# Performance work log

Measured on AMD Instinct MI355X. Metric: run time of the kernel, lower is better.

## Reference

```python
import jax, jax.numpy as jnp
import numpy as np
import itertools


def _interpn_linear(vol, loc):
    """Trilinear interpolation of vol [D,H,W,C] at absolute coords loc [D,H,W,3].
    Matches neurite's interpn: clip coords to volume, floor/ceil corners, 8-corner
    weighted sum (nearest-extrapolation at borders)."""
    D, H, W, C = vol.shape
    max_idx = jnp.asarray([D - 1, H - 1, W - 1], dtype=loc.dtype)
    loc = jnp.clip(loc, 0.0, max_idx)
    loc0 = jnp.floor(loc)
    loc1 = jnp.minimum(loc0 + 1.0, max_idx)
    d1 = loc1 - loc                     # weight of corner 0 (floor)
    d0 = 1.0 - d1                       # weight of corner 1 (ceil)
    w = jnp.stack([d1, d0], axis=0)     # [2, D,H,W,3]
    idx = jnp.stack([loc0, loc1], axis=0).astype(jnp.int32)  # [2, D,H,W,3]
    vol_flat = vol.reshape(-1, C)
    out = jnp.zeros(loc.shape[:-1] + (C,), vol.dtype)
    for c in itertools.product((0, 1), repeat=3):  # fixed 8-corner loop
        flat = (idx[c[0], ..., 0] * H + idx[c[1], ..., 1]) * W + idx[c[2], ..., 2]
        wt = w[c[0], ..., 0] * w[c[1], ..., 1] * w[c[2], ..., 2]
        out = out + wt[..., None] * vol_flat[flat]
    return out


def _warp(vol, shift):
    """Sample dense field vol [D,H,W,3] at grid + shift (voxelmorph transform())."""
    D, H, W, _ = shift.shape
    grid = jnp.stack(
        jnp.meshgrid(jnp.arange(D), jnp.arange(H), jnp.arange(W), indexing='ij'),
        axis=-1,
    ).astype(shift.dtype)
    return _interpn_linear(vol, grid + shift)


def _compose(transforms):
    """voxelmorph utils.compose for dense transforms: T(x) = C(B(A(x))).
    curr = curr + warp(nxt, curr), folding right-to-left."""
    curr = transforms[-1]
    for nxt in reversed(transforms[:-1]):
        curr = curr + jax.vmap(_warp)(nxt, curr)
    return curr


def setup_inputs() -> dict:
    key = jax.random.key(0)
    k1, k2, k3 = jax.random.split(key, 3)
    shape = (2, 128, 160, 192, 3)  # [B, D, H, W, ndims] dense displacement fields
    scale = 3.0  # ~3-voxel displacements, realistic registration magnitude
    return {
        't1': scale * jax.random.normal(k1, shape, dtype=jnp.float32),
        't2': scale * jax.random.normal(k2, shape, dtype=jnp.float32),
        't3': scale * jax.random.normal(k3, shape, dtype=jnp.float32),
    }


def reference(t1, t2, t3):
    # Transforms listed in application order A, B, C -> T(x) = C(B(A(x)))
    return _compose([t1, t2, t3])
```

## Files before the change

### kernel.cpp

```cpp
#include <hip/hip_runtime.h>
#include <hip/hip_fp16.h>


#define BB 2
#define DD 128
#define HH 160
#define WW 192

#define WT_TILES 3
#define HT_TILES 80
#define DT_TILES 64
#define NBLOCKS (WT_TILES * HT_TILES * DT_TILES * BB)
#define PER_XCD (NBLOCKS / 8)

static __device__ __forceinline__ float3 cvt_h4(uint2 q) {
    float2 fa = __half22float2(*(const __half2*)&q.x);
    float  fz = __half2float(*(const __half*)&q.y);
    return make_float3(fa.x, fa.y, fz);
}

__global__ __launch_bounds__(256) void conv_f16_kernel(
    const float* __restrict__ src, uint2* __restrict__ dst)
{
    long i = (long)blockIdx.x * blockDim.x + threadIdx.x;
    const float4* s4 = (const float4*)src;
    float4 A = s4[3 * i], B = s4[3 * i + 1], C = s4[3 * i + 2];

    float v[4][3] = {{A.x, A.y, A.z}, {A.w, B.x, B.y},
                     {B.z, B.w, C.x}, {C.y, C.z, C.w}};
#pragma unroll
    for (int j = 0; j < 4; ++j) {
        unsigned short hx = __half_as_ushort(__float2half_rn(v[j][0]));
        unsigned short hy = __half_as_ushort(__float2half_rn(v[j][1]));
        unsigned short hz = __half_as_ushort(__float2half_rn(v[j][2]));
        uint2 q;
        q.x = (unsigned)hx | ((unsigned)hy << 16);
        q.y = (unsigned)hz;
        dst[4 * i + j] = q;
    }
}

__global__ __launch_bounds__(256) void warp_add_h_kernel(
    const uint2* __restrict__ vol4,
    const float* shift,
    float* out)
{
    unsigned bid  = blockIdx.x;
    unsigned sbid = (bid & 7u) * PER_XCD + (bid >> 3);

    unsigned wt  = sbid % WT_TILES;  unsigned t0 = sbid / WT_TILES;
    unsigned ht  = t0 % HT_TILES;    unsigned t1 = t0 / HT_TILES;
    unsigned dt  = t1 % DT_TILES;    unsigned b  = t1 / DT_TILES;

    unsigned tid = threadIdx.x;
    int w = wt * 64 + (tid & 63);
    int h = ht * 2  + ((tid >> 6) & 1);
    int d = dt * 2  + (tid >> 7);

    const long nvb = (long)DD * HH * WW;
    long idx = (long)b * nvb + (((long)d * HH + h) * WW + w);

    const float* sp = shift + idx * 3;
    float sx = sp[0], sy = sp[1], sz = sp[2];

    float lx = fminf(fmaxf((float)d + sx, 0.f), (float)(DD - 1));
    float ly = fminf(fmaxf((float)h + sy, 0.f), (float)(HH - 1));
    float lz = fminf(fmaxf((float)w + sz, 0.f), (float)(WW - 1));

    float fx = floorf(lx), fy = floorf(ly), fz = floorf(lz);
    int x0 = (int)fx, y0 = (int)fy, z0 = (int)fz;
    int x1 = min(x0 + 1, DD - 1);
    int y1 = min(y0 + 1, HH - 1);

    int  z0m = min(z0, WW - 2);
    bool zhi = (z0 == WW - 1);

    float wx0 = (float)x1 - lx;
    float wy0 = (float)y1 - ly;
    float wz0 = (float)(min(z0 + 1, WW - 1)) - lz;
    float wx1 = 1.f - wx0;
    float wy1 = 1.f - wy0;
    float wz1 = 1.f - wz0;

    const uint2* baseq = vol4 + (long)b * nvb;

    float ax = 0.f, ay = 0.f, az = 0.f;
#define ROWPAIR(X, Y, WXY) do {                                             \
        const uint2* pp = baseq + (((long)(X) * HH + (Y)) * WW + z0m);      \
        uint2 qlo = pp[0], qhi = pp[1];                    \
        float3 vlo = cvt_h4(qlo), vhi = cvt_h4(qhi);                        \
        float3 v0  = zhi ? vhi : vlo;                                       \
        float wt_ = (WXY);                                                  \
        ax = fmaf(wt_, fmaf(wz0, v0.x, wz1 * vhi.x), ax);                   \
        ay = fmaf(wt_, fmaf(wz0, v0.y, wz1 * vhi.y), ay);                   \
        az = fmaf(wt_, fmaf(wz0, v0.z, wz1 * vhi.z), az);                   \
    } while (0)

    ROWPAIR(x0, y0, wx0 * wy0);
    ROWPAIR(x0, y1, wx0 * wy1);
    ROWPAIR(x1, y0, wx1 * wy0);
    ROWPAIR(x1, y1, wx1 * wy1);
#undef ROWPAIR

    float* op = out + idx * 3;
    op[0] = sx + ax;
    op[1] = sy + ay;
    op[2] = sz + az;
}

extern "C" void kernel_launch(void* const* d_in, const int* in_sizes, int n_in,
                              void* d_out, int out_size, void* d_ws, size_t ws_size,
                              hipStream_t stream) {
    const float* t1 = (const float*)d_in[0];
    const float* t2 = (const float*)d_in[1];
    const float* t3 = (const float*)d_in[2];
    float* out  = (float*)d_out;
    uint2* volh = (uint2*)d_ws;

    const long nvt = (long)BB * DD * HH * WW;
    const int  conv_blocks = (int)(nvt / 4 / 256);

    conv_f16_kernel<<<conv_blocks, 256, 0, stream>>>(t2, volh);
    warp_add_h_kernel<<<NBLOCKS, 256, 0, stream>>>(volh, t3, out);
    conv_f16_kernel<<<conv_blocks, 256, 0, stream>>>(t1, volh);
    warp_add_h_kernel<<<NBLOCKS, 256, 0, stream>>>(volh, out, out);
}
```

Baseline: 598.8 us.

## Stage f16 conversion through LDS and process two voxels per warp thread

The conversion kernel now loads float4s cooperatively into shared memory and writes coalesced uint2 outputs per thread, replacing strided 48-byte-per-thread loads and 4-stride stores. The warp kernel now handles two adjacent W voxels per thread, with shift loads and output stores done as float2, and all eight gather loads issued up front before any arithmetic to raise memory-level parallelism. The D tile is halved to keep the grid mapping consistent. The cost is higher register pressure and an LDS sync in the conversion kernel.

```diff
diff --git a/kernel.cpp b/kernel.cpp
--- a/kernel.cpp
+++ b/kernel.cpp
@@ -9,7 +9,7 @@
 
 #define WT_TILES 3
 #define HT_TILES 80
-#define DT_TILES 64
+#define DT_TILES 32
 #define NBLOCKS (WT_TILES * HT_TILES * DT_TILES * BB)
 #define PER_XCD (NBLOCKS / 8)
 
@@ -20,49 +20,36 @@
 }
 
 __global__ __launch_bounds__(256) void conv_f16_kernel(
-    const float* __restrict__ src, uint2* __restrict__ dst)
+    const float4* __restrict__ src, uint2* __restrict__ dst)
 {
-    long i = (long)blockIdx.x * blockDim.x + threadIdx.x;
-    const float4* s4 = (const float4*)src;
-    float4 A = s4[3 * i], B = s4[3 * i + 1], C = s4[3 * i + 2];
+    __shared__ float4 lds4[768];
+    const float* lds = (const float*)lds4;
 
-    float v[4][3] = {{A.x, A.y, A.z}, {A.w, B.x, B.y},
-                     {B.z, B.w, C.x}, {C.y, C.z, C.w}};
+    long base = (long)blockIdx.x * 1024;
+    const float4* s4 = src + (long)blockIdx.x * 768;
+    int tid = threadIdx.x;
+
+#pragma unroll
+    for (int j = 0; j < 3; ++j)
+        lds4[tid + 256 * j] = s4[tid + 256 * j];
+    __syncthreads();
+
 #pragma unroll
     for (int j = 0; j < 4; ++j) {
-        unsigned short hx = __half_as_ushort(__float2half_rn(v[j][0]));
-        unsigned short hy = __half_as_ushort(__float2half_rn(v[j][1]));
-        unsigned short hz = __half_as_ushort(__float2half_rn(v[j][2]));
+        int v = tid + 256 * j;
+        float x = lds[3 * v], y = lds[3 * v + 1], z = lds[3 * v + 2];
         uint2 q;
-        q.x = (unsigned)hx | ((unsigned)hy << 16);
-        q.y = (unsigned)hz;
-        dst[4 * i + j] = q;
+        q.x = (unsigned)__half_as_ushort(__float2half_rn(x)) |
+              ((unsigned)__half_as_ushort(__float2half_rn(y)) << 16);
+        q.y = (unsigned)__half_as_ushort(__float2half_rn(z));
+        dst[base + v] = q;
     }
 }
 
-__global__ __launch_bounds__(256) void warp_add_h_kernel(
-    const uint2* __restrict__ vol4,
-    const float* shift,
-    float* out)
+static __device__ __forceinline__ void interp_one(
+    const uint2* __restrict__ baseq, int d, int h, int w,
+    float sx, float sy, float sz, float& ox, float& oy, float& oz)
 {
-    unsigned bid  = blockIdx.x;
-    unsigned sbid = (bid & 7u) * PER_XCD + (bid >> 3);
-
-    unsigned wt  = sbid % WT_TILES;  unsigned t0 = sbid / WT_TILES;
-    unsigned ht  = t0 % HT_TILES;    unsigned t1 = t0 / HT_TILES;
-    unsigned dt  = t1 % DT_TILES;    unsigned b  = t1 / DT_TILES;
-
-    unsigned tid = threadIdx.x;
-    int w = wt * 64 + (tid & 63);
-    int h = ht * 2  + ((tid >> 6) & 1);
-    int d = dt * 2  + (tid >> 7);
-
-    const long nvb = (long)DD * HH * WW;
-    long idx = (long)b * nvb + (((long)d * HH + h) * WW + w);
-
-    const float* sp = shift + idx * 3;
-    float sx = sp[0], sy = sp[1], sz = sp[2];
-
     float lx = fminf(fmaxf((float)d + sx, 0.f), (float)(DD - 1));
     float ly = fminf(fmaxf((float)h + sy, 0.f), (float)(HH - 1));
     float lz = fminf(fmaxf((float)w + sz, 0.f), (float)(WW - 1));
@@ -82,30 +69,68 @@
     float wy1 = 1.f - wy0;
     float wz1 = 1.f - wz0;
 
-    const uint2* baseq = vol4 + (long)b * nvb;
+    const uint2* p00 = baseq + (((long)x0 * HH + y0) * WW + z0m);
+    const uint2* p01 = baseq + (((long)x0 * HH + y1) * WW + z0m);
+    const uint2* p10 = baseq + (((long)x1 * HH + y0) * WW + z0m);
+    const uint2* p11 = baseq + (((long)x1 * HH + y1) * WW + z0m);
+    uint2 q00l = p00[0], q00h = p00[1];
+    uint2 q01l = p01[0], q01h = p01[1];
+    uint2 q10l = p10[0], q10h = p10[1];
+    uint2 q11l = p11[0], q11h = p11[1];
 
     float ax = 0.f, ay = 0.f, az = 0.f;
-#define ROWPAIR(X, Y, WXY) do {                                             \
-        const uint2* pp = baseq + (((long)(X) * HH + (Y)) * WW + z0m);      \
-        uint2 qlo = pp[0], qhi = pp[1];                    \
-        float3 vlo = cvt_h4(qlo), vhi = cvt_h4(qhi);                        \
+#define ROWPAIR(QL, QH, WXY) do {                                           \
+        float3 vlo = cvt_h4(QL), vhi = cvt_h4(QH);                          \
         float3 v0  = zhi ? vhi : vlo;                                       \
         float wt_ = (WXY);                                                  \
         ax = fmaf(wt_, fmaf(wz0, v0.x, wz1 * vhi.x), ax);                   \
         ay = fmaf(wt_, fmaf(wz0, v0.y, wz1 * vhi.y), ay);                   \
         az = fmaf(wt_, fmaf(wz0, v0.z, wz1 * vhi.z), az);                   \
     } while (0)
-
-    ROWPAIR(x0, y0, wx0 * wy0);
-    ROWPAIR(x0, y1, wx0 * wy1);
-    ROWPAIR(x1, y0, wx1 * wy0);
-    ROWPAIR(x1, y1, wx1 * wy1);
+    ROWPAIR(q00l, q00h, wx0 * wy0);
+    ROWPAIR(q01l, q01h, wx0 * wy1);
+    ROWPAIR(q10l, q10h, wx1 * wy0);
+    ROWPAIR(q11l, q11h, wx1 * wy1);
 #undef ROWPAIR
 
-    float* op = out + idx * 3;
-    op[0] = sx + ax;
-    op[1] = sy + ay;
-    op[2] = sz + az;
+    ox = sx + ax;
+    oy = sy + ay;
+    oz = sz + az;
+}
+
+__global__ __launch_bounds__(256) void warp_add_h_kernel(
+    const uint2* __restrict__ vol4,
+    const float* shift,
+    float* out)
+{
+    unsigned bid  = blockIdx.x;
+    unsigned sbid = (bid & 7u) * PER_XCD + (bid >> 3);
+
+    unsigned wt  = sbid % WT_TILES;  unsigned t0 = sbid / WT_TILES;
+    unsigned ht  = t0 % HT_TILES;    unsigned t1 = t0 / HT_TILES;
+    unsigned dt  = t1 % DT_TILES;    unsigned b  = t1 / DT_TILES;
+
+    unsigned tid = threadIdx.x;
+    int w = wt * 64 + 2 * (tid & 31);
+    int h = ht * 2  + ((tid >> 5) & 1);
+    int d = dt * 4  + (tid >> 6);
+
+    const long nvb = (long)DD * HH * WW;
+    long idx = (long)b * nvb + (((long)d * HH + h) * WW + w);
+
+    const float2* sp2 = (const float2*)(shift + idx * 3);
+    float2 sa = sp2[0], sb = sp2[1], sc = sp2[2];
+
+    const uint2* baseq = vol4 + (long)b * nvb;
+
+    float o0x, o0y, o0z, o1x, o1y, o1z;
+    interp_one(baseq, d, h, w,     sa.x, sa.y, sb.x, o0x, o0y, o0z);
+    interp_one(baseq, d, h, w + 1, sb.y, sc.x, sc.y, o1x, o1y, o1z);
+
+    float2* op2 = (float2*)(out + idx * 3);
+    op2[0] = make_float2(o0x, o0y);
+    op2[1] = make_float2(o0z, o1x);
+    op2[2] = make_float2(o1y, o1z);
 }
 
 extern "C" void kernel_launch(void* const* d_in, const int* in_sizes, int n_in,
@@ -118,10 +143,10 @@
     uint2* volh = (uint2*)d_ws;
 
     const long nvt = (long)BB * DD * HH * WW;
-    const int  conv_blocks = (int)(nvt / 4 / 256);
+    const int  conv_blocks = (int)(nvt / 1024);
 
-    conv_f16_kernel<<<conv_blocks, 256, 0, stream>>>(t2, volh);
+    conv_f16_kernel<<<conv_blocks, 256, 0, stream>>>((const float4*)t2, volh);
     warp_add_h_kernel<<<NBLOCKS, 256, 0, stream>>>(volh, t3, out);
-    conv_f16_kernel<<<conv_blocks, 256, 0, stream>>>(t1, volh);
+    conv_f16_kernel<<<conv_blocks, 256, 0, stream>>>((const float4*)t1, volh);
     warp_add_h_kernel<<<NBLOCKS, 256, 0, stream>>>(volh, out, out);
 }
```

Result: faster. 578.5 us (-3.4%).
